# Kernel tuning notes

Measured on AMD Instinct MI355X. Metric: run time of the kernel, lower is better.

Reference implementation:

```python
import jax, jax.numpy as jnp
import numpy as np
from jax import lax

ENC_DIM, DEC_DIM, ATT_DIM, CONV_CH, KSIZE, ATT_ODIM = 1024, 1024, 512, 32, 50, 1024
SCALING = 2.0


def setup_inputs() -> dict:
    key = jax.random.key(0)
    ks = jax.random.split(key, 12)
    B, T = 32, 2000
    enc_pad = jax.random.normal(ks[0], (B, T, ENC_DIM), dtype=jnp.float32)
    enc_len = jax.random.randint(ks[1], (B,), 1000, T + 1, dtype=jnp.int32)
    dec_h = jax.random.normal(ks[2], (B, 1, DEC_DIM), dtype=jnp.float32)
    att_prev = jax.random.uniform(ks[3], (B, T), dtype=jnp.float32)
    s = 0.02
    W_enc = jax.random.normal(ks[4], (ENC_DIM, ATT_DIM), dtype=jnp.float32) * s
    b_enc = jnp.zeros((ATT_DIM,), jnp.float32)
    W_dec = jax.random.normal(ks[5], (DEC_DIM, ATT_DIM), dtype=jnp.float32) * s
    b_dec = jnp.zeros((ATT_DIM,), jnp.float32)
    W_att = jax.random.normal(ks[6], (CONV_CH, ATT_DIM), dtype=jnp.float32) * s
    b_att = jnp.zeros((ATT_DIM,), jnp.float32)
    # Conv2d(1, C, kernel=(1, 2K+1)) acting on (B,1,1,T) == 1D conv kernel (C,1,2K+1)
    conv_w = jax.random.normal(ks[7], (CONV_CH, 1, 2 * KSIZE + 1), dtype=jnp.float32) * s
    gvec = jax.random.normal(ks[8], (ATT_DIM, 1), dtype=jnp.float32) * s
    W_o = jax.random.normal(ks[9], (ENC_DIM, ATT_ODIM), dtype=jnp.float32) * s
    b_o = jnp.zeros((ATT_ODIM,), jnp.float32)
    return {"enc_pad": enc_pad, "enc_len": enc_len, "dec_h": dec_h, "att_prev": att_prev,
            "W_enc": W_enc, "b_enc": b_enc, "W_dec": W_dec, "b_dec": b_dec,
            "W_att": W_att, "b_att": b_att, "conv_w": conv_w, "gvec": gvec,
            "W_o": W_o, "b_o": b_o}


def reference(enc_pad, enc_len, dec_h, att_prev, W_enc, b_enc, W_dec, b_dec,
              W_att, b_att, conv_w, gvec, W_o, b_o):
    B, T, _ = enc_pad.shape
    enc_h = enc_pad @ W_enc + b_enc                           # [B,T,A]
    # location conv: (B,1,T) * (C,1,K) -> (B,C,T), SAME padding
    att_conv = lax.conv_general_dilated(
        att_prev[:, None, :], conv_w, window_strides=(1,),
        padding=[(KSIZE, KSIZE)], dimension_numbers=("NCH", "OIH", "NCH"))
    att_conv = jnp.transpose(att_conv, (0, 2, 1)) @ W_att + b_att  # [B,T,A]
    dec_term = (dec_h.reshape(B, DEC_DIM) @ W_dec + b_dec)[:, None, :]  # [B,1,A]
    att_state = jnp.tanh(enc_h + dec_term + att_conv)         # [B,T,A]
    e = (att_state @ gvec)[:, :, 0]                           # [B,T]
    mask = jnp.arange(T)[None, :] >= enc_len[:, None]         # True = padded
    e = jnp.where(mask, jnp.float32(-1e15), e)
    attn = jax.nn.softmax(SCALING * e, axis=1)                # [B,T]
    c = jnp.einsum("bt,btd->bd", attn, enc_pad)               # [B,enc_dim]
    c = c @ W_o + b_o                                         # [B,att_odim]
    return c, attn
```

## Files before the change

### kernel.cpp

```cpp
#include <hip/hip_runtime.h>
#include <stdint.h>
#include <stddef.h>

#define T_LEN   2000
#define BATCH   32
#define ROWS    64000
#define KDIM    1024
#define ADIM    512
#define CCH     32
#define KW      101

typedef _Float16 half8_t  __attribute__((ext_vector_type(8)));
typedef _Float16 half4_t  __attribute__((ext_vector_type(4)));
typedef float    float4_t __attribute__((ext_vector_type(4)));

__device__ __forceinline__ half8_t pack8(float4_t a, float4_t b) {
    half8_t r;
    r[0] = (_Float16)a.x; r[1] = (_Float16)a.y;
    r[2] = (_Float16)a.z; r[3] = (_Float16)a.w;
    r[4] = (_Float16)b.x; r[5] = (_Float16)b.y;
    r[6] = (_Float16)b.z; r[7] = (_Float16)b.w;
    return r;
}

__device__ __forceinline__ float tanh_fast(float x) {
    float ax = __builtin_fabsf(x);
    ax = fminf(ax, 15.f);
    float e = __expf(2.f * ax);
    float t = 1.f - 2.f * __builtin_amdgcn_rcpf(e + 1.f);
    return (x < 0.f) ? -t : t;
}

__device__ __forceinline__ void glds16(const void* g, void* l) {
    __builtin_amdgcn_global_load_lds((const __attribute__((address_space(1))) uint32_t*)g,
                                     (__attribute__((address_space(3))) uint32_t*)l,
                                     16, 0, 0);
}

#define OFF_WENCT 0
#define OFF_WATTT 1048576
#define OFF_CONV  1081344
#define M_DTERM   5177344
#define M_EPART   5242880
#define M_CPART   6266880
#define M_ENCH    8364032
#define F_DTERM   9273344
#define F_EPART   9338880
#define F_CPART   10362880

__global__ __launch_bounds__(256) void k_prep(const float* __restrict__ We,
                                              const float* __restrict__ Wa,
                                              const float* __restrict__ dec_h,
                                              const float* __restrict__ W_dec,
                                              const float* __restrict__ be,
                                              const float* __restrict__ bd,
                                              const float* __restrict__ ba,
                                              const float* __restrict__ att_prev,
                                              const float* __restrict__ conv_w,
                                              const float* __restrict__ enc,
                                              _Float16* __restrict__ Wet,
                                              _Float16* __restrict__ Wat,
                                              float* __restrict__ dterm,
                                              void* __restrict__ convO,
                                              _Float16* __restrict__ encH,
                                              int f16mode) {
    __shared__ float smem[3460];
    const int blk = blockIdx.x, tid = threadIdx.x;

    if (blk >= 1153) {
        const size_t base = (size_t)(blk - 1153) * 8192 + (size_t)tid * 8;
#pragma unroll
        for (int i = 0; i < 4; ++i) {
            const size_t idx = base + (size_t)i * 2048;
            const float4_t* s = (const float4_t*)(enc + idx);
            *(half8_t*)(encH + idx) = pack8(s[0], s[1]);
        }
        return;
    }
    if (blk < 512) {
        float (*tile)[33] = (float(*)[33])smem;
        const int k0 = (blk >> 4) * 32, n0 = (blk & 15) * 32;
        const int tx = tid & 31, ty = tid >> 5;
#pragma unroll
        for (int i = 0; i < 4; ++i)
            tile[ty + i * 8][tx] = We[(size_t)(k0 + ty + i * 8) * ADIM + n0 + tx];
        __syncthreads();
#pragma unroll
        for (int i = 0; i < 4; ++i)
            Wet[(size_t)(n0 + ty + i * 8) * KDIM + k0 + tx] = (_Float16)tile[tx][ty + i * 8];
    } else if (blk < 640) {
        float* dh = smem;
        float* part = smem + 1024;
        const int idx = blk - 512, b = idx >> 2, a0 = (idx & 3) * 128;
#pragma unroll
        for (int i = 0; i < 4; ++i) dh[tid + i * 256] = dec_h[b * KDIM + tid + i * 256];
        __syncthreads();
        const int a = a0 + (tid & 127), kh = (tid >> 7) * 512;
        float s = 0.f;
#pragma unroll 8
        for (int k = 0; k < 512; ++k) s += dh[kh + k] * W_dec[(size_t)(kh + k) * ADIM + a];
        part[tid] = s;
        __syncthreads();
        if (tid < 128) {
            const int aa = a0 + tid;
            dterm[b * ADIM + aa] = part[tid] + part[tid + 128] + be[aa] + bd[aa] + ba[aa];
        }
    } else if (blk < 1152) {
        float* ap = smem;
        float* w  = smem + 228;
        const int idx = blk - 640, b = idx >> 4, tt = idx & 15;
        const int t0 = tt * 128;
        for (int i = tid; i < 228; i += 256) {
            int t = t0 - 50 + i;
            ap[i] = (t >= 0 && t < T_LEN) ? att_prev[b * T_LEN + t] : 0.f;
        }
        for (int i = tid; i < CCH * KW; i += 256) w[i] = conv_w[i];
        __syncthreads();
        for (int idx2 = tid; idx2 < 128 * CCH; idx2 += 256) {
            int tl = idx2 >> 5, c = idx2 & 31;
            int t = t0 + tl;
            if (t < T_LEN) {
                float s = 0.f;
#pragma unroll
                for (int j = 0; j < KW; ++j) s += ap[tl + j] * w[c * KW + j];
                const size_t o = (size_t)(b * T_LEN + t) * CCH + c;
                if (f16mode) ((_Float16*)convO)[o] = (_Float16)s;
                else         ((float*)convO)[o] = s;
            }
        }
    } else {
#pragma unroll
        for (int rr = 0; rr < 2; ++rr) {
            const int n = tid * 2 + rr;
#pragma unroll
            for (int c = 0; c < CCH; ++c)
                Wat[n * CCH + c] = (_Float16)Wa[c * ADIM + n];
        }
    }
}

__global__ __launch_bounds__(256, 3)
void k_gemm3(const _Float16* __restrict__ encH,
             const _Float16* __restrict__ Wet,
             const _Float16* __restrict__ cvH,
             const _Float16* __restrict__ Wat,
             const float* __restrict__ dterm,
             const float* __restrict__ gvec,
             float* __restrict__ epart) {
    __shared__ __attribute__((aligned(16))) char     Ab[3][8192];
    __shared__ __attribute__((aligned(16))) _Float16 Bh[3][4096];

    const int tid  = threadIdx.x;
    const int blk  = blockIdx.x;
    int nc, mt;
    if (blk < 1984) { nc = (blk >> 3) & 3; mt = (blk >> 5) * 8 + (blk & 7); }
    else            { int r = blk - 1984; nc = r >> 2; mt = 496 + (r & 3); }
    const int m0 = mt * 128, n0 = nc * 128;

    const int wave = tid >> 6, lane = tid & 63;
    const int quad = lane >> 4, c16 = lane & 15;
    const int wm = (wave >> 1) * 64, wn = (wave & 1) * 64;
    const int rl = lane & 15, sg = lane >> 4;

    const size_t aRow = (size_t)(m0 + wave * 32 + rl);
    const size_t bRow = (size_t)(n0 + wave * 32 + rl);

    float g[4], dt0[4], dt1[4];
    const int b0 = m0 / T_LEN, b1 = (m0 + 127) / T_LEN;
    const int lim = (b0 + 1) * T_LEN;
#pragma unroll
    for (int j = 0; j < 4; ++j) {
        const int col = n0 + wn + j * 16 + c16;
        g[j]   = gvec[col];
        dt0[j] = dterm[b0 * ADIM + col];
        dt1[j] = dterm[b1 * ADIM + col];
    }

    float4_t acc[4][4];
#pragma unroll
    for (int i = 0; i < 4; ++i)
#pragma unroll
        for (int j = 0; j < 4; ++j) acc[i][j] = (float4_t){0.f, 0.f, 0.f, 0.f};

#define STG(bf, s)                                                                  \
    {                                                                               \
        if ((s) < 32) {                                                             \
            const int kn = (s) * 32;                                                \
            _Pragma("unroll")                                                       \
            for (int i = 0; i < 2; ++i)                                             \
                glds16(encH + (aRow + (size_t)(i * 16)) * KDIM + kn + sg * 8,       \
                       &Ab[bf][(wave * 2 + i) * 1024]);                             \
            _Pragma("unroll")                                                       \
            for (int i = 0; i < 2; ++i)                                             \
                glds16(Wet + (bRow + (size_t)(i * 16)) * KDIM + kn + sg * 8,        \
                       (char*)&Bh[bf][0] + (wave * 2 + i) * 1024);                  \
        } else {                                                                    \
            _Pragma("unroll")                                                       \
            for (int i = 0; i < 2; ++i)                                             \
                glds16(cvH + (aRow + (size_t)(i * 16)) * CCH + sg * 8,              \
                       &Ab[bf][(wave * 2 + i) * 1024]);                             \
            _Pragma("unroll")                                                       \
            for (int i = 0; i < 2; ++i)                                             \
                glds16(Wat + (bRow + (size_t)(i * 16)) * CCH + sg * 8,              \
                       (char*)&Bh[bf][0] + (wave * 2 + i) * 1024);                  \
        }                                                                           \
    }

    STG(0, 0)
    STG(1, 1)

    for (int kk = 0; kk < 33; ++kk) {
        if (kk < 32) asm volatile("s_waitcnt vmcnt(4)" ::: "memory");
        else         asm volatile("s_waitcnt vmcnt(0)" ::: "memory");
        __builtin_amdgcn_s_barrier();
        __builtin_amdgcn_sched_barrier(0);

        const int s = kk + 2;
        if (s <= 32) { const int bf = s - (s / 3) * 3; STG(bf, s) }

        const int cur = kk - (kk / 3) * 3;
        const _Float16* Ah = (const _Float16*)Ab[cur];
        const _Float16* Bp = &Bh[cur][0];
        half8_t af[4], bf4[4];
#pragma unroll
        for (int i = 0; i < 4; ++i)
            af[i] = *(const half8_t*)(Ah + ((wm + i * 16) >> 4) * 512 + lane * 8);
#pragma unroll
        for (int j = 0; j < 4; ++j)
            bf4[j] = *(const half8_t*)(Bp + ((wn + j * 16) >> 4) * 512 + lane * 8);
#pragma unroll
        for (int i = 0; i < 4; ++i)
#pragma unroll
            for (int j = 0; j < 4; ++j)
                acc[i][j] = __builtin_amdgcn_mfma_f32_16x16x32_f16(af[i], bf4[j], acc[i][j], 0, 0, 0);
    }
#undef STG
    __syncthreads();

    float* e_lds = (float*)&Bh[0][0];
#pragma unroll
    for (int i = 0; i < 4; ++i) {
#pragma unroll
        for (int r = 0; r < 4; ++r) {
            const int rloc = wm + i * 16 + quad * 4 + r;
            const bool hi = (m0 + rloc) >= lim;
            float s = 0.f;
#pragma unroll
            for (int j = 0; j < 4; ++j)
                s += tanh_fast(acc[i][j][r] + (hi ? dt1[j] : dt0[j])) * g[j];
#pragma unroll
            for (int off = 1; off < 16; off <<= 1) s += __shfl_xor(s, off);
            if (c16 == 0) e_lds[rloc * 2 + (wave & 1)] = s;
        }
    }
    __syncthreads();
    if (tid < 128) {
        const float2 q = ((const float2*)e_lds)[tid];
        epart[nc * ROWS + m0 + tid] = q.x + q.y;
    }
}

__global__ __launch_bounds__(256, 3)
void k_gemm_f(const float* __restrict__ encF,
              const _Float16* __restrict__ Wet,
              const float* __restrict__ cvF,
              const _Float16* __restrict__ Wat,
              const float* __restrict__ dterm,
              const float* __restrict__ gvec,
              float* __restrict__ epart) {
    __shared__ __attribute__((aligned(16))) char     Ab[2][16384];
    __shared__ __attribute__((aligned(16))) _Float16 Bh[2][128 * 32];

    const int tid  = threadIdx.x;
    const int blk  = blockIdx.x;
    int nc, mt;
    if (blk < 1984) { nc = (blk >> 3) & 3; mt = (blk >> 5) * 8 + (blk & 7); }
    else            { int r = blk - 1984; nc = r >> 2; mt = 496 + (r & 3); }
    const int m0 = mt * 128, n0 = nc * 128;

    const int wave = tid >> 6, lane = tid & 63;
    const int quad = lane >> 4, c16 = lane & 15;
    const int wm = (wave >> 1) * 64, wn = (wave & 1) * 64;

    const int rlB = lane & 15, sgB = lane >> 4;
    const int rlA = lane & 7,  sgA = lane >> 3;

    const size_t aRow = (size_t)(m0 + wave * 32 + rlA);
    const size_t bRow = (size_t)(n0 + wave * 32 + rlB);

    float g[4], dt0[4], dt1[4];
    const int b0 = m0 / T_LEN, b1 = (m0 + 127) / T_LEN;
    const int lim = (b0 + 1) * T_LEN;
#pragma unroll
    for (int j = 0; j < 4; ++j) {
        const int col = n0 + wn + j * 16 + c16;
        g[j]   = gvec[col];
        dt0[j] = dterm[b0 * ADIM + col];
        dt1[j] = dterm[b1 * ADIM + col];
    }

    float4_t acc[4][4];
#pragma unroll
    for (int i = 0; i < 4; ++i)
#pragma unroll
        for (int j = 0; j < 4; ++j) acc[i][j] = (float4_t){0.f, 0.f, 0.f, 0.f};

#define STAGE_A(buf, base, stride, k0)                                              \
    _Pragma("unroll")                                                               \
    for (int i = 0; i < 4; ++i)                                                     \
        glds16((base) + ((aRow + i * 8) * (stride)) + (k0) + sgA * 4,               \
               &Ab[buf][(wave * 4 + i) * 1024]);
#define STAGE_B(buf, base, stride, k0)                                              \
    _Pragma("unroll")                                                               \
    for (int i = 0; i < 2; ++i)                                                     \
        glds16((base) + ((bRow + i * 16) * (stride)) + (k0) + sgB * 8,              \
               (char*)&Bh[buf][0] + (wave * 2 + i) * 1024);

    STAGE_A(0, encF, KDIM, 0)
    STAGE_B(0, Wet, KDIM, 0)
    __syncthreads();

    for (int kk = 0; kk < 33; ++kk) {
        const int cur = kk & 1, nxt = cur ^ 1;
        if (kk < 31) {
            const int kn = (kk + 1) * 32;
            STAGE_A(nxt, encF, KDIM, kn)
            STAGE_B(nxt, Wet, KDIM, kn)
        } else if (kk == 31) {
            STAGE_A(nxt, cvF, CCH, 0)
            STAGE_B(nxt, Wat, CCH, 0)
        }
        half8_t af[4], bf[4];
        const float* Afp = (const float*)Ab[cur];
#pragma unroll
        for (int i = 0; i < 4; ++i) {
            const int row = wm + i * 16 + c16;
            const float* cb = Afp + (row >> 3) * 256 + (row & 7) * 4;
            float4_t u0 = *(const float4_t*)(cb + (2 * quad) * 32);
            float4_t u1 = *(const float4_t*)(cb + (2 * quad + 1) * 32);
            af[i] = pack8(u0, u1);
        }
#pragma unroll
        for (int j = 0; j < 4; ++j) {
            const int row = wn + j * 16 + c16;
            bf[j] = *(const half8_t*)(&Bh[cur][0] + (row >> 4) * 512 + (quad * 16 + c16) * 8);
        }
#pragma unroll
        for (int i = 0; i < 4; ++i)
#pragma unroll
            for (int j = 0; j < 4; ++j)
                acc[i][j] = __builtin_amdgcn_mfma_f32_16x16x32_f16(af[i], bf[j], acc[i][j], 0, 0, 0);
        __syncthreads();
    }
#undef STAGE_A
#undef STAGE_B

    float* e_lds = (float*)&Bh[0][0];
#pragma unroll
    for (int i = 0; i < 4; ++i) {
#pragma unroll
        for (int r = 0; r < 4; ++r) {
            const int rloc = wm + i * 16 + quad * 4 + r;
            const bool hi = (m0 + rloc) >= lim;
            float s = 0.f;
#pragma unroll
            for (int j = 0; j < 4; ++j)
                s += tanh_fast(acc[i][j][r] + (hi ? dt1[j] : dt0[j])) * g[j];
#pragma unroll
            for (int off = 1; off < 16; off <<= 1) s += __shfl_xor(s, off);
            if (c16 == 0) e_lds[rloc * 2 + (wave & 1)] = s;
        }
    }
    __syncthreads();
    if (tid < 128) {
        const float2 q = ((const float2*)e_lds)[tid];
        epart[nc * ROWS + m0 + tid] = q.x + q.y;
    }
}

__global__ __launch_bounds__(512) void k_softmax(const float* __restrict__ epart,
                                                 const int* __restrict__ enc_len,
                                                 float* __restrict__ attn) {
    __shared__ float ex[T_LEN];
    __shared__ float red[8];
    const int b = blockIdx.x, tid = threadIdx.x;
    const int len = enc_len[b];
    float lmax = -3.4e38f;
    for (int t = tid; t < T_LEN; t += 512) {
        float e = epart[b * T_LEN + t] + epart[ROWS + b * T_LEN + t]
                + epart[2 * ROWS + b * T_LEN + t] + epart[3 * ROWS + b * T_LEN + t];
        float lg = (t < len) ? 2.f * e : -2e15f;
        ex[t] = lg;
        lmax = fmaxf(lmax, lg);
    }
    for (int off = 1; off < 64; off <<= 1) lmax = fmaxf(lmax, __shfl_xor(lmax, off));
    if ((tid & 63) == 0) red[tid >> 6] = lmax;
    __syncthreads();
    const float m = fmaxf(fmaxf(fmaxf(red[0], red[1]), fmaxf(red[2], red[3])),
                          fmaxf(fmaxf(red[4], red[5]), fmaxf(red[6], red[7])));
    float lsum = 0.f;
    for (int t = tid; t < T_LEN; t += 512) {
        float p = __expf(ex[t] - m);
        ex[t] = p;
        lsum += p;
    }
    for (int off = 1; off < 64; off <<= 1) lsum += __shfl_xor(lsum, off);
    __syncthreads();
    if ((tid & 63) == 0) red[tid >> 6] = lsum;
    __syncthreads();
    const float inv = 1.f / (red[0] + red[1] + red[2] + red[3] + red[4] + red[5] + red[6] + red[7]);
    for (int t = tid; t < T_LEN; t += 512) attn[b * T_LEN + t] = ex[t] * inv;
}

__global__ __launch_bounds__(256) void k_cpart_h(const float* __restrict__ attn,
                                                 const _Float16* __restrict__ encH,
                                                 float* __restrict__ cpart) {
    const int b = blockIdx.y, tc = blockIdx.x, tid = threadIdx.x;
    const int t0 = tc * 125;
    float4_t s = (float4_t){0.f, 0.f, 0.f, 0.f};
    const half4_t* ep = (const half4_t*)(encH + (size_t)b * T_LEN * KDIM) + tid;
    const float* ap = attn + b * T_LEN + t0;
#pragma unroll 5
    for (int tt = 0; tt < 125; ++tt) {
        const float w = ap[tt];
        half4_t v = ep[(size_t)(t0 + tt) * 256];
        s.x += w * (float)v[0]; s.y += w * (float)v[1];
        s.z += w * (float)v[2]; s.w += w * (float)v[3];
    }
    *(float4_t*)&cpart[(size_t)(tc * BATCH + b) * KDIM + tid * 4] = s;
}

__global__ __launch_bounds__(256) void k_cpart_f(const float* __restrict__ attn,
                                                 const float* __restrict__ enc,
                                                 float* __restrict__ cpart) {
    const int b = blockIdx.y, tc = blockIdx.x, tid = threadIdx.x;
    const int t0 = tc * 125;
    float4_t s = (float4_t){0.f, 0.f, 0.f, 0.f};
    const float4_t* ep = (const float4_t*)(enc + (size_t)b * T_LEN * KDIM) + tid;
    const float* ap = attn + b * T_LEN + t0;
#pragma unroll 5
    for (int tt = 0; tt < 125; ++tt) {
        const float w = ap[tt];
        float4_t v = ep[(size_t)(t0 + tt) * 256];
        s += v * w;
    }
    *(float4_t*)&cpart[(size_t)(tc * BATCH + b) * KDIM + tid * 4] = s;
}

__global__ __launch_bounds__(256) void k_out(const float* __restrict__ cpart,
                                             const float* __restrict__ W_o,
                                             const float* __restrict__ b_o,
                                             float* __restrict__ out_c) {
    __shared__ float cm[KDIM];
    const int b = blockIdx.x, tid = threadIdx.x;
    for (int d = tid; d < KDIM; d += 256) {
        float s = 0.f;
#pragma unroll
        for (int p = 0; p < 16; ++p) s += cpart[(size_t)(p * BATCH + b) * KDIM + d];
        cm[d] = s;
    }
    __syncthreads();
    const int o = blockIdx.y * 256 + tid;
    float s = b_o[o];
#pragma unroll 8
    for (int d = 0; d < KDIM; ++d) s += cm[d] * W_o[(size_t)d * KDIM + o];
    out_c[b * KDIM + o] = s;
}

extern "C" void kernel_launch(void* const* d_in, const int* in_sizes, int n_in,
                              void* d_out, int out_size, void* d_ws, size_t ws_size,
                              hipStream_t stream) {
    const float* enc      = (const float*)d_in[0];
    const int*   enc_len  = (const int*)d_in[1];
    const float* dec_h    = (const float*)d_in[2];
    const float* att_prev = (const float*)d_in[3];
    const float* W_enc    = (const float*)d_in[4];
    const float* b_enc    = (const float*)d_in[5];
    const float* W_dec    = (const float*)d_in[6];
    const float* b_dec    = (const float*)d_in[7];
    const float* W_att    = (const float*)d_in[8];
    const float* b_att    = (const float*)d_in[9];
    const float* conv_w   = (const float*)d_in[10];
    const float* gvec     = (const float*)d_in[11];
    const float* W_o      = (const float*)d_in[12];
    const float* b_o      = (const float*)d_in[13];

    float* out_c    = (float*)d_out;
    float* out_attn = out_c + BATCH * KDIM;

    char* ws = (char*)d_ws;
    _Float16* Wet = (_Float16*)(ws + OFF_WENCT);
    _Float16* Wat = (_Float16*)(ws + OFF_WATTT);

    const size_t needMain = (size_t)M_ENCH + (size_t)ROWS * KDIM * 2;
    const bool f16p = ws_size >= needMain;

    if (f16p) {
        _Float16* convH = (_Float16*)(ws + OFF_CONV);
        float*    dterm = (float*)(ws + M_DTERM);
        float*    epart = (float*)(ws + M_EPART);
        float*    cpart = (float*)(ws + M_CPART);
        _Float16* encH  = (_Float16*)(ws + M_ENCH);

        k_prep<<<1153 + 8000, 256, 0, stream>>>(W_enc, W_att, dec_h, W_dec, b_enc, b_dec,
                                                b_att, att_prev, conv_w, enc,
                                                Wet, Wat, dterm, convH, encH, 1);
        k_gemm3<<<2000, 256, 0, stream>>>(encH, Wet, convH, Wat, dterm, gvec, epart);
        k_softmax<<<BATCH, 512, 0, stream>>>(epart, enc_len, out_attn);
        k_cpart_h<<<dim3(16, BATCH), 256, 0, stream>>>(out_attn, encH, cpart);
        k_out<<<dim3(BATCH, 4), 256, 0, stream>>>(cpart, W_o, b_o, out_c);
    } else {
        float* convF = (float*)(ws + OFF_CONV);
        float* dterm = (float*)(ws + F_DTERM);
        float* epart = (float*)(ws + F_EPART);
        float* cpart = (float*)(ws + F_CPART);

        k_prep<<<1153, 256, 0, stream>>>(W_enc, W_att, dec_h, W_dec, b_enc, b_dec,
                                         b_att, att_prev, conv_w, enc,
                                         Wet, Wat, dterm, convF, (_Float16*)nullptr, 0);
        k_gemm_f<<<2000, 256, 0, stream>>>(enc, Wet, convF, Wat, dterm, gvec, epart);
        k_softmax<<<BATCH, 512, 0, stream>>>(epart, enc_len, out_attn);
        k_cpart_f<<<dim3(16, BATCH), 256, 0, stream>>>(out_attn, enc, cpart);
        k_out<<<dim3(BATCH, 4), 256, 0, stream>>>(cpart, W_o, b_o, out_c);
    }
}
```

Before: 637.0 us.

## Widen fp16 GEMM tile to 128x256 with 512 threads and double buffering

Replaces the 128x128 triple-buffered GEMM kernel with a 128x256 tile run by 8 waves per block, so each encoder row tile is loaded once per two column halves instead of four. The grid halves to 1000 blocks and softmax now sums two partial-score planes instead of four. The pipeline drops from three LDS stages with partial vmcnt waits to two stages with a full __syncthreads per k-step. That gives up some load/compute overlap in exchange for less A-operand traffic and fewer epart partials.

```diff
diff --git a/kernel.cpp b/kernel.cpp
--- a/kernel.cpp
+++ b/kernel.cpp
@@ -139,31 +139,32 @@
     }
 }
 
-__global__ __launch_bounds__(256, 3)
-void k_gemm3(const _Float16* __restrict__ encH,
-             const _Float16* __restrict__ Wet,
-             const _Float16* __restrict__ cvH,
-             const _Float16* __restrict__ Wat,
-             const float* __restrict__ dterm,
-             const float* __restrict__ gvec,
-             float* __restrict__ epart) {
-    __shared__ __attribute__((aligned(16))) char     Ab[3][8192];
-    __shared__ __attribute__((aligned(16))) _Float16 Bh[3][4096];
+__global__ __launch_bounds__(512, 6)
+void k_gemm_h(const _Float16* __restrict__ encH,
+              const _Float16* __restrict__ Wet,
+              const _Float16* __restrict__ cvH,
+              const _Float16* __restrict__ Wat,
+              const float* __restrict__ dterm,
+              const float* __restrict__ gvec,
+              float* __restrict__ epart) {
+    __shared__ __attribute__((aligned(16))) char Ab[2][8192];
+    __shared__ __attribute__((aligned(16))) char Bh[2][16384];
 
     const int tid  = threadIdx.x;
     const int blk  = blockIdx.x;
     int nc, mt;
-    if (blk < 1984) { nc = (blk >> 3) & 3; mt = (blk >> 5) * 8 + (blk & 7); }
-    else            { int r = blk - 1984; nc = r >> 2; mt = 496 + (r & 3); }
-    const int m0 = mt * 128, n0 = nc * 128;
+    if (blk < 992) { nc = (blk >> 3) & 1; mt = (blk >> 4) * 8 + (blk & 7); }
+    else           { int r = blk - 992; nc = r >> 2; mt = 496 + (r & 3); }
+    const int m0 = mt * 128, n0 = nc * 256;
 
     const int wave = tid >> 6, lane = tid & 63;
     const int quad = lane >> 4, c16 = lane & 15;
-    const int wm = (wave >> 1) * 64, wn = (wave & 1) * 64;
+    const int wm = (wave >> 2) * 64, wn = (wave & 3) * 64;
     const int rl = lane & 15, sg = lane >> 4;
 
-    const size_t aRow = (size_t)(m0 + wave * 32 + rl);
-    const size_t bRow = (size_t)(n0 + wave * 32 + rl);
+    const size_t aRow  = (size_t)(m0 + wave * 16 + rl);
+    const size_t bRow0 = (size_t)(n0 + (2 * wave) * 16 + rl);
+    const size_t bRow1 = bRow0 + 16;
 
     float g[4], dt0[4], dt1[4];
     const int b0 = m0 / T_LEN, b1 = (m0 + 127) / T_LEN;
@@ -182,62 +183,41 @@
 #pragma unroll
         for (int j = 0; j < 4; ++j) acc[i][j] = (float4_t){0.f, 0.f, 0.f, 0.f};
 
-#define STG(bf, s)                                                                  \
-    {                                                                               \
-        if ((s) < 32) {                                                             \
-            const int kn = (s) * 32;                                                \
-            _Pragma("unroll")                                                       \
-            for (int i = 0; i < 2; ++i)                                             \
-                glds16(encH + (aRow + (size_t)(i * 16)) * KDIM + kn + sg * 8,       \
-                       &Ab[bf][(wave * 2 + i) * 1024]);                             \
-            _Pragma("unroll")                                                       \
-            for (int i = 0; i < 2; ++i)                                             \
-                glds16(Wet + (bRow + (size_t)(i * 16)) * KDIM + kn + sg * 8,        \
-                       (char*)&Bh[bf][0] + (wave * 2 + i) * 1024);                  \
-        } else {                                                                    \
-            _Pragma("unroll")                                                       \
-            for (int i = 0; i < 2; ++i)                                             \
-                glds16(cvH + (aRow + (size_t)(i * 16)) * CCH + sg * 8,              \
-                       &Ab[bf][(wave * 2 + i) * 1024]);                             \
-            _Pragma("unroll")                                                       \
-            for (int i = 0; i < 2; ++i)                                             \
-                glds16(Wat + (bRow + (size_t)(i * 16)) * CCH + sg * 8,              \
-                       (char*)&Bh[bf][0] + (wave * 2 + i) * 1024);                  \
-        }                                                                           \
-    }
-
-    STG(0, 0)
-    STG(1, 1)
+#define STG(bf, Abase, Bbase, stride, kn)                                          \
+    glds16((Abase) + aRow  * (stride) + (kn) + sg * 8, &Ab[bf][wave * 1024]);      \
+    glds16((Bbase) + bRow0 * (stride) + (kn) + sg * 8, &Bh[bf][(2 * wave) * 1024]);\
+    glds16((Bbase) + bRow1 * (stride) + (kn) + sg * 8, &Bh[bf][(2 * wave + 1) * 1024]);
+
+    STG(0, encH, Wet, KDIM, 0)
+    __syncthreads();
 
     for (int kk = 0; kk < 33; ++kk) {
-        if (kk < 32) asm volatile("s_waitcnt vmcnt(4)" ::: "memory");
-        else         asm volatile("s_waitcnt vmcnt(0)" ::: "memory");
-        __builtin_amdgcn_s_barrier();
-        __builtin_amdgcn_sched_barrier(0);
-
-        const int s = kk + 2;
-        if (s <= 32) { const int bf = s - (s / 3) * 3; STG(bf, s) }
-
-        const int cur = kk - (kk / 3) * 3;
+        const int cur = kk & 1, nxt = cur ^ 1;
+        if (kk < 31) {
+            const int kn = (kk + 1) * 32;
+            STG(nxt, encH, Wet, KDIM, kn)
+        } else if (kk == 31) {
+            STG(nxt, cvH, Wat, CCH, 0)
+        }
+        half8_t af[4], bf4[4];
         const _Float16* Ah = (const _Float16*)Ab[cur];
-        const _Float16* Bp = &Bh[cur][0];
-        half8_t af[4], bf4[4];
+        const _Float16* Bp = (const _Float16*)Bh[cur];
 #pragma unroll
         for (int i = 0; i < 4; ++i)
-            af[i] = *(const half8_t*)(Ah + ((wm + i * 16) >> 4) * 512 + lane * 8);
+            af[i] = *(const half8_t*)(Ah + (wm / 16 + i) * 512 + lane * 8);
 #pragma unroll
         for (int j = 0; j < 4; ++j)
-            bf4[j] = *(const half8_t*)(Bp + ((wn + j * 16) >> 4) * 512 + lane * 8);
+            bf4[j] = *(const half8_t*)(Bp + (wn / 16 + j) * 512 + lane * 8);
 #pragma unroll
         for (int i = 0; i < 4; ++i)
 #pragma unroll
             for (int j = 0; j < 4; ++j)
                 acc[i][j] = __builtin_amdgcn_mfma_f32_16x16x32_f16(af[i], bf4[j], acc[i][j], 0, 0, 0);
+        __syncthreads();
     }
 #undef STG
-    __syncthreads();
-
-    float* e_lds = (float*)&Bh[0][0];
+
+    float* e_lds = (float*)Bh[0];
 #pragma unroll
     for (int i = 0; i < 4; ++i) {
 #pragma unroll
@@ -250,13 +230,13 @@
                 s += tanh_fast(acc[i][j][r] + (hi ? dt1[j] : dt0[j])) * g[j];
 #pragma unroll
             for (int off = 1; off < 16; off <<= 1) s += __shfl_xor(s, off);
-            if (c16 == 0) e_lds[rloc * 2 + (wave & 1)] = s;
+            if (c16 == 0) e_lds[rloc * 4 + (wave & 3)] = s;
         }
     }
     __syncthreads();
     if (tid < 128) {
-        const float2 q = ((const float2*)e_lds)[tid];
-        epart[nc * ROWS + m0 + tid] = q.x + q.y;
+        const float4_t q = ((const float4_t*)e_lds)[tid];
+        epart[nc * ROWS + m0 + tid] = q.x + q.y + q.z + q.w;
     }
 }
 
@@ -380,15 +360,16 @@
 
 __global__ __launch_bounds__(512) void k_softmax(const float* __restrict__ epart,
                                                  const int* __restrict__ enc_len,
-                                                 float* __restrict__ attn) {
+                                                 float* __restrict__ attn,
+                                                 int np) {
     __shared__ float ex[T_LEN];
     __shared__ float red[8];
     const int b = blockIdx.x, tid = threadIdx.x;
     const int len = enc_len[b];
     float lmax = -3.4e38f;
     for (int t = tid; t < T_LEN; t += 512) {
-        float e = epart[b * T_LEN + t] + epart[ROWS + b * T_LEN + t]
-                + epart[2 * ROWS + b * T_LEN + t] + epart[3 * ROWS + b * T_LEN + t];
+        float e = epart[b * T_LEN + t];
+        for (int p = 1; p < np; ++p) e += epart[p * ROWS + b * T_LEN + t];
         float lg = (t < len) ? 2.f * e : -2e15f;
         ex[t] = lg;
         lmax = fmaxf(lmax, lg);
@@ -505,8 +486,8 @@
         k_prep<<<1153 + 8000, 256, 0, stream>>>(W_enc, W_att, dec_h, W_dec, b_enc, b_dec,
                                                 b_att, att_prev, conv_w, enc,
                                                 Wet, Wat, dterm, convH, encH, 1);
-        k_gemm3<<<2000, 256, 0, stream>>>(encH, Wet, convH, Wat, dterm, gvec, epart);
-        k_softmax<<<BATCH, 512, 0, stream>>>(epart, enc_len, out_attn);
+        k_gemm_h<<<1000, 512, 0, stream>>>(encH, Wet, convH, Wat, dterm, gvec, epart);
+        k_softmax<<<BATCH, 512, 0, stream>>>(epart, enc_len, out_attn, 2);
         k_cpart_h<<<dim3(16, BATCH), 256, 0, stream>>>(out_attn, encH, cpart);
         k_out<<<dim3(BATCH, 4), 256, 0, stream>>>(cpart, W_o, b_o, out_c);
     } else {
@@ -519,7 +500,7 @@
                                          b_att, att_prev, conv_w, enc,
                                          Wet, Wat, dterm, convF, (_Float16*)nullptr, 0);
         k_gemm_f<<<2000, 256, 0, stream>>>(enc, Wet, convF, Wat, dterm, gvec, epart);
-        k_softmax<<<BATCH, 512, 0, stream>>>(epart, enc_len, out_attn);
+        k_softmax<<<BATCH, 512, 0, stream>>>(epart, enc_len, out_attn, 4);
         k_cpart_f<<<dim3(16, BATCH), 256, 0, stream>>>(out_attn, enc, cpart);
         k_out<<<dim3(BATCH, 4), 256, 0, stream>>>(cpart, W_o, b_o, out_c);
     }
```

After: 954.9 us. +49.9%, slower.
